# Performance work log

Hardware: AMD Instinct MI355X
Metric: run time of the kernel (lower is better)

Reference implementation:

```python
import jax, jax.numpy as jnp
import numpy as np

# Dimensions: classic FORCE setup (Sussillo & Abbott / tension EchoStateNetwork)
N = 1024      # force_layer.units (reservoir size)
T = 128       # timesteps (train_step loops over x.shape[1])
I_DIM = 16    # input dimension
O_DIM = 8     # output dimension
DT = 0.1      # leak rate of the reservoir cell
ALPHA_P = 1.0 # P initialized to alpha_P * I (keras.initializers.Identity(gain=alpha_P))


def setup_inputs() -> dict:
    key = jax.random.key(0)
    k0, k1, k2, k3, k4 = jax.random.split(key, 5)
    x = jax.random.normal(k0, (1, T, I_DIM), dtype=jnp.float32)
    y = jax.random.normal(k1, (1, T, O_DIM), dtype=jnp.float32)
    Win = jax.random.normal(k2, (I_DIM, N), dtype=jnp.float32) * (1.0 / np.sqrt(I_DIM))
    # spectral-radius-style scaling keeps the reservoir in the chaotic-edge regime
    Wrec = jax.random.normal(k3, (N, N), dtype=jnp.float32) * (1.5 / np.sqrt(N))
    Wfb = jax.random.normal(k4, (O_DIM, N), dtype=jnp.float32)
    wO = jnp.zeros((N, O_DIM), dtype=jnp.float32)        # output_kernel starts at 0
    P = ALPHA_P * jnp.eye(N, dtype=jnp.float32)           # P_output = alpha_P * I
    return {"x": x, "y": y, "Win": Win, "Wrec": Wrec, "Wfb": Wfb, "wO": wO, "P": P}


def reference(x, y, Win, Wrec, Wfb, wO, P):
    """FORCEModel.train_step: per-timestep RNN forward + RLS (FORCE) update.

    Per step t (batch is fixed to 1, so states are vectors):
      a_t = (1-dt)*a_{t-1} + dt*(h_{t-1}@Wrec + x_t@Win + z_{t-1}@Wfb)
      h_t = tanh(a_t);  z_t = h_t @ wO   (output uses wO *before* this step's update)
      RLS (pseudogradient_P, SGD lr=1 => P -= dP):
        k = P @ h;  c = 1/(1 + h.k);  P <- P - c * k k^T
      then (pseudogradient_wO with the *updated* P, matching apply_gradients order):
        e = z - y_t;  wO <- wO - (P @ h) e^T
    Returns the sequence of pre-update outputs z_t, shape (T, O_DIM).
    """
    xs = x[0]  # (T, I_DIM)
    ys = y[0]  # (T, O_DIM)
    a0 = jnp.zeros((N,), dtype=x.dtype)
    h0 = jnp.tanh(a0)
    z0 = jnp.zeros((O_DIM,), dtype=x.dtype)

    def step(carry, inp):
        a, h, z, P_t, wO_t = carry
        xt, yt = inp
        a = (1.0 - DT) * a + DT * (h @ Wrec + xt @ Win + z @ Wfb)
        h = jnp.tanh(a)
        z = h @ wO_t                           # (O_DIM,)
        # pseudogradient_P: rank-1 Sherman-Morrison style update of P
        k = P_t @ h                            # (N,)
        c = 1.0 / (1.0 + jnp.dot(h, k))
        P_t = P_t - c * jnp.outer(k, k)
        # pseudogradient_wO with updated P
        wO_t = wO_t - jnp.outer(P_t @ h, z - yt)
        return (a, h, z, P_t, wO_t), z

    (_, _, _, P_f, wO_f), zs = jax.lax.scan(step, (a0, h0, z0, P, wO), (xs, ys))
    return zs  # (T, O_DIM)
```

## Files before the change

### kernel.cpp

```cpp
#include <hip/hip_runtime.h>
#include <math.h>


#define NN   1024
#define TT   128
#define IDIM 16
#define ODIM 8
#define NBLK 64
#define NTHR 256
#define JPB  16
#define GST  (TT + 8)
#define NGRP 8
#define WREC_LD (NN + 4)

#define AL(p)    __hip_atomic_load((p), __ATOMIC_RELAXED, __HIP_MEMORY_SCOPE_AGENT)
#define AS(p, v) __hip_atomic_store((p), (v), __ATOMIC_RELAXED, __HIP_MEMORY_SCOPE_AGENT)

struct WS {
  unsigned arrive[NGRP][32];
  unsigned master[32];
  unsigned rel[NGRP][32];
  float hglob[2][NN];
  float gpart[2][NBLK][GST];
};

__global__ __launch_bounds__(NTHR, 1) void force_rls_kernel(
    const float* __restrict__ x, const float* __restrict__ y,
    const float* __restrict__ Win, const float* __restrict__ Wrec,
    const float* __restrict__ Wfb, float* __restrict__ out, WS* ws)
{
  const int tid  = threadIdx.x;
  const int bid  = blockIdx.x;
  const int lane = tid & 63;
  const int wv   = tid >> 6;
  const int j0   = bid * JPB;
  const int jj   = tid & 15;
  const int qq   = tid >> 4;
  const int grp  = bid >> 3;

  __shared__ float Wsl_t[JPB][WREC_LD];
  __shared__ float Ksl[TT][JPB];
  __shared__ float XW[TT][JPB];
  __shared__ float Ybuf[TT][ODIM];
  __shared__ float Ebuf[TT][ODIM];
  __shared__ float hfull[NN];
  __shared__ float cbuf[TT], dbuf[TT];
  __shared__ float Wfb_s[ODIM][JPB];
  __shared__ float Winsl[IDIM][JPB];
  __shared__ float redK[16][JPB], redM[16][JPB];
  __shared__ float redG[2][TT];
  __shared__ float hcb[JPB], abuf[JPB], zbuf[ODIM];
  __shared__ float red2[4];
  __shared__ float sHH;

  for (int m = 0; m < (NN * JPB) / NTHR; ++m) {
    int e = m * NTHR + tid;
    int r = e >> 4, j = e & 15;
    Wsl_t[j][r] = Wrec[(size_t)r * NN + j0 + j];
  }
  { int i = tid >> 4, j = tid & 15; Winsl[i][j] = Win[i * NN + j0 + j]; }
  if (tid < ODIM * JPB) { int o = tid >> 4, j = tid & 15; Wfb_s[o][j] = Wfb[o * NN + j0 + j]; }
  for (int m = 0; m < (TT * ODIM) / NTHR; ++m) {
    int e = m * NTHR + tid; Ybuf[e >> 3][e & 7] = y[e];
  }
  if (tid < JPB) abuf[tid] = 0.f;
  if (tid < ODIM) zbuf[tid] = 0.f;
  __syncthreads();
  for (int m = 0; m < (TT * JPB) / NTHR; ++m) {
    int e = m * NTHR + tid; int t = e >> 4, j = e & 15;
    float s = 0.f;
#pragma unroll
    for (int i = 0; i < IDIM; ++i) s += x[t * IDIM + i] * Winsl[i][j];
    XW[t][j] = s;
  }
  __syncthreads();

  for (int t = 0; t < TT; ++t) {
    const int p = t & 1;

    if (t >= 1) {
      const float* hg = ws->hglob[p ^ 1];
#pragma unroll
      for (int m = 0; m < NN / NTHR; ++m) {
        int idx = m * NTHR + tid;
        hfull[idx] = AL(&hg[idx]);
      }
    }
    __syncthreads();

    float kp = 0.f;
    if (t >= 1) {
      for (int s = qq; s < t - 1; s += 16) kp -= dbuf[s] * Ksl[s][jj];
    }
    redK[qq][jj] = kp;

    float mp = 0.f;
    if (t >= 1) {
      const float4* hf4 = (const float4*)hfull;
#pragma unroll
      for (int i = 0; i < 16; ++i) {
        const int rb = (i << 6) + (qq << 2);
        const float4 w  = *(const float4*)&Wsl_t[jj][rb];
        const float4 hv = hf4[rb >> 2];
        mp += hv.x * w.x + hv.y * w.y + hv.z * w.z + hv.w * w.w;
      }
    }
    redM[qq][jj] = mp;
    __syncthreads();

    if (tid < JPB) {
      const int j = tid;
      if (t >= 1) {
        float kv = hfull[j0 + j];
#pragma unroll
        for (int q = 0; q < 16; ++q) kv += redK[q][j];
        Ksl[t - 1][j] = kv;
      }
      float acc = 0.f;
#pragma unroll
      for (int q = 0; q < 16; ++q) acc += redM[q][j];
      float fb = 0.f;
#pragma unroll
      for (int o = 0; o < ODIM; ++o) fb += zbuf[o] * Wfb_s[o][j];
      float a = 0.9f * abuf[j] + 0.1f * (acc + XW[t][j] + fb);
      abuf[j] = a;
      float h = tanhf(a);
      hcb[j] = h;
      AS(&ws->hglob[p][j0 + j], h);
    }
    __syncthreads();

    if (tid <= t) {
      float gp = 0.f;
      if (tid < t) {
#pragma unroll
        for (int j = 0; j < JPB; ++j) gp += Ksl[tid][j] * hcb[j];
      } else {
#pragma unroll
        for (int j = 0; j < JPB; ++j) gp += hcb[j] * hcb[j];
      }
      AS(&ws->gpart[p][bid][tid], gp);
    }

    __syncthreads();
    if (tid == 0) {
      asm volatile("s_waitcnt vmcnt(0)" ::: "memory");
      const unsigned tgt = (unsigned)(t + 1) * 8u;
      unsigned r = __hip_atomic_fetch_add(&ws->arrive[grp][0], 1u,
                      __ATOMIC_RELAXED, __HIP_MEMORY_SCOPE_AGENT);
      if (r == tgt - 1u) {
        unsigned m = __hip_atomic_fetch_add(&ws->master[0], 1u,
                        __ATOMIC_RELAXED, __HIP_MEMORY_SCOPE_AGENT);
        if (m == tgt - 1u) {
#pragma unroll
          for (int g = 0; g < NGRP; ++g) AS(&ws->rel[g][0], (unsigned)(t + 1));
        }
      }
      while (AL(&ws->rel[grp][0]) < (unsigned)(t + 1))
        __builtin_amdgcn_s_sleep(8);
      asm volatile("s_waitcnt vmcnt(0)" ::: "memory");
    }
    __syncthreads();

    {
      const int sF = tid & 127;
      const int hf = tid >> 7;
      float gp = 0.f;
      if (sF <= t) {
        const int b0 = hf * 32;
#pragma unroll
        for (int b = 0; b < 32; ++b) gp += AL(&ws->gpart[p][b0 + b][sF]);
      }
      redG[hf][sF] = gp;
    }
    __syncthreads();
    float dval = 0.f, gval = 0.f;
    if (tid <= t) {
      float g = redG[0][tid] + redG[1][tid];
      gval = g;
      if (tid < t) { dval = cbuf[tid] * g; dbuf[tid] = dval; }
      else sHH = g;
    }
    float s1p = dval * gval;
    s1p += __shfl_xor(s1p, 1, 64);
    s1p += __shfl_xor(s1p, 2, 64);
    s1p += __shfl_xor(s1p, 4, 64);
    s1p += __shfl_xor(s1p, 8, 64);
    s1p += __shfl_xor(s1p, 16, 64);
    s1p += __shfl_xor(s1p, 32, 64);
    if (lane == 0) red2[wv] = s1p;
    __syncthreads();
    if (tid == 0) {
      float s1 = red2[0] + red2[1] + red2[2] + red2[3];
      cbuf[t] = 1.f / (1.f + sHH - s1);
    }
    if (wv == 0) {
      const int o = lane & 7, gr8 = lane >> 3;
      float zp = 0.f;
      for (int s = gr8; s < t; s += 8) zp += dbuf[s] * Ebuf[s][o];
      zp += __shfl_xor(zp, 8, 64);
      zp += __shfl_xor(zp, 16, 64);
      zp += __shfl_xor(zp, 32, 64);
      if (lane < 8) {
        float z = -zp;
        zbuf[o] = z;
        Ebuf[t][o] = z - Ybuf[t][o];
        if (bid == 0) out[t * ODIM + o] = z;
      }
    }
    __syncthreads();
  }
}

extern "C" void kernel_launch(void* const* d_in, const int* in_sizes, int n_in,
                              void* d_out, int out_size, void* d_ws, size_t ws_size,
                              hipStream_t stream) {
  const float* x    = (const float*)d_in[0];
  const float* y    = (const float*)d_in[1];
  const float* Win  = (const float*)d_in[2];
  const float* Wrec = (const float*)d_in[3];
  const float* Wfb  = (const float*)d_in[4];
  float* out = (float*)d_out;
  WS* ws = (WS*)d_ws;

  hipMemsetAsync(d_ws, 0, sizeof(unsigned) * 32 * (NGRP * 2 + 1), stream);
  force_rls_kernel<<<NBLK, NTHR, 0, stream>>>(x, y, Win, Wrec, Wfb, out, ws);
}
```

Baseline: 806.7 us.

## Merge grid barriers into one per step via flag array and deferred reduction

```diff
diff --git a/kernel.cpp b/kernel.cpp
--- a/kernel.cpp
+++ b/kernel.cpp
@@ -10,16 +10,13 @@
 #define NTHR 256
 #define JPB  16
 #define GST  (TT + 8)
-#define NGRP 8
 #define WREC_LD (NN + 4)
 
 #define AL(p)    __hip_atomic_load((p), __ATOMIC_RELAXED, __HIP_MEMORY_SCOPE_AGENT)
 #define AS(p, v) __hip_atomic_store((p), (v), __ATOMIC_RELAXED, __HIP_MEMORY_SCOPE_AGENT)
 
 struct WS {
-  unsigned arrive[NGRP][32];
-  unsigned master[32];
-  unsigned rel[NGRP][32];
+  unsigned flag[64];
   float hglob[2][NN];
   float gpart[2][NBLK][GST];
 };
@@ -36,7 +33,8 @@
   const int j0   = bid * JPB;
   const int jj   = tid & 15;
   const int qq   = tid >> 4;
-  const int grp  = bid >> 3;
+  const int sF   = tid & 127;
+  const int hf   = tid >> 7;
 
   __shared__ float Wsl_t[JPB][WREC_LD];
   __shared__ float Ksl[TT][JPB];
@@ -80,19 +78,23 @@
 
     if (t >= 1) {
       const float* hg = ws->hglob[p ^ 1];
-#pragma unroll
-      for (int m = 0; m < NN / NTHR; ++m) {
-        int idx = m * NTHR + tid;
-        hfull[idx] = AL(&hg[idx]);
-      }
-    }
-    __syncthreads();
-
-    float kp = 0.f;
-    if (t >= 1) {
-      for (int s = qq; s < t - 1; s += 16) kp -= dbuf[s] * Ksl[s][jj];
-    }
-    redK[qq][jj] = kp;
+      float hr0 = AL(&hg[tid]);
+      float hr1 = AL(&hg[NTHR + tid]);
+      float hr2 = AL(&hg[2 * NTHR + tid]);
+      float hr3 = AL(&hg[3 * NTHR + tid]);
+      float ga = 0.f;
+      if (sF < t) {
+        const float* gq = &ws->gpart[p ^ 1][hf * 32][sF];
+#pragma unroll
+        for (int b = 0; b < 32; ++b) ga += AL(&gq[b * GST]);
+      }
+      hfull[tid]            = hr0;
+      hfull[NTHR + tid]     = hr1;
+      hfull[2 * NTHR + tid] = hr2;
+      hfull[3 * NTHR + tid] = hr3;
+      redG[hf][sF] = ga;
+    }
+    __syncthreads();
 
     float mp = 0.f;
     if (t >= 1) {
@@ -106,79 +108,12 @@
       }
     }
     redM[qq][jj] = mp;
-    __syncthreads();
-
-    if (tid < JPB) {
-      const int j = tid;
-      if (t >= 1) {
-        float kv = hfull[j0 + j];
-#pragma unroll
-        for (int q = 0; q < 16; ++q) kv += redK[q][j];
-        Ksl[t - 1][j] = kv;
-      }
-      float acc = 0.f;
-#pragma unroll
-      for (int q = 0; q < 16; ++q) acc += redM[q][j];
-      float fb = 0.f;
-#pragma unroll
-      for (int o = 0; o < ODIM; ++o) fb += zbuf[o] * Wfb_s[o][j];
-      float a = 0.9f * abuf[j] + 0.1f * (acc + XW[t][j] + fb);
-      abuf[j] = a;
-      float h = tanhf(a);
-      hcb[j] = h;
-      AS(&ws->hglob[p][j0 + j], h);
-    }
-    __syncthreads();
-
-    if (tid <= t) {
-      float gp = 0.f;
-      if (tid < t) {
-#pragma unroll
-        for (int j = 0; j < JPB; ++j) gp += Ksl[tid][j] * hcb[j];
-      } else {
-#pragma unroll
-        for (int j = 0; j < JPB; ++j) gp += hcb[j] * hcb[j];
-      }
-      AS(&ws->gpart[p][bid][tid], gp);
-    }
-
-    __syncthreads();
-    if (tid == 0) {
-      asm volatile("s_waitcnt vmcnt(0)" ::: "memory");
-      const unsigned tgt = (unsigned)(t + 1) * 8u;
-      unsigned r = __hip_atomic_fetch_add(&ws->arrive[grp][0], 1u,
-                      __ATOMIC_RELAXED, __HIP_MEMORY_SCOPE_AGENT);
-      if (r == tgt - 1u) {
-        unsigned m = __hip_atomic_fetch_add(&ws->master[0], 1u,
-                        __ATOMIC_RELAXED, __HIP_MEMORY_SCOPE_AGENT);
-        if (m == tgt - 1u) {
-#pragma unroll
-          for (int g = 0; g < NGRP; ++g) AS(&ws->rel[g][0], (unsigned)(t + 1));
-        }
-      }
-      while (AL(&ws->rel[grp][0]) < (unsigned)(t + 1))
-        __builtin_amdgcn_s_sleep(8);
-      asm volatile("s_waitcnt vmcnt(0)" ::: "memory");
-    }
-    __syncthreads();
-
-    {
-      const int sF = tid & 127;
-      const int hf = tid >> 7;
-      float gp = 0.f;
-      if (sF <= t) {
-        const int b0 = hf * 32;
-#pragma unroll
-        for (int b = 0; b < 32; ++b) gp += AL(&ws->gpart[p][b0 + b][sF]);
-      }
-      redG[hf][sF] = gp;
-    }
-    __syncthreads();
+
     float dval = 0.f, gval = 0.f;
-    if (tid <= t) {
+    if (t >= 1 && tid <= t - 1) {
       float g = redG[0][tid] + redG[1][tid];
       gval = g;
-      if (tid < t) { dval = cbuf[tid] * g; dbuf[tid] = dval; }
+      if (tid < t - 1) { dval = cbuf[tid] * g; dbuf[tid] = dval; }
       else sHH = g;
     }
     float s1p = dval * gval;
@@ -190,25 +125,104 @@
     s1p += __shfl_xor(s1p, 32, 64);
     if (lane == 0) red2[wv] = s1p;
     __syncthreads();
+
+    if (t >= 1) {
+      if (tid == 0) {
+        float s1 = red2[0] + red2[1] + red2[2] + red2[3];
+        cbuf[t - 1] = 1.f / (1.f + sHH - s1);
+      }
+      if (wv == 0) {
+        const int o = lane & 7, gr8 = lane >> 3;
+        float zp = 0.f;
+        for (int s = gr8; s < t - 1; s += 8) zp += dbuf[s] * Ebuf[s][o];
+        zp += __shfl_xor(zp, 8, 64);
+        zp += __shfl_xor(zp, 16, 64);
+        zp += __shfl_xor(zp, 32, 64);
+        if (lane < 8) {
+          float z = -zp;
+          zbuf[o] = z;
+          Ebuf[t - 1][o] = z - Ybuf[t - 1][o];
+          if (bid == 0) out[(t - 1) * ODIM + o] = z;
+        }
+      }
+    }
+    float kp = 0.f;
+    if (t >= 2) {
+      for (int s = qq; s < t - 1; s += 16) kp -= dbuf[s] * Ksl[s][jj];
+    }
+    redK[qq][jj] = kp;
+    __syncthreads();
+
+    if (tid < JPB) {
+      const int j = tid;
+      if (t >= 1) {
+        float kv = hfull[j0 + j];
+#pragma unroll
+        for (int q = 0; q < 16; ++q) kv += redK[q][j];
+        Ksl[t - 1][j] = kv;
+      }
+      float acc = 0.f;
+#pragma unroll
+      for (int q = 0; q < 16; ++q) acc += redM[q][j];
+      float fb = 0.f;
+#pragma unroll
+      for (int o = 0; o < ODIM; ++o) fb += zbuf[o] * Wfb_s[o][j];
+      float a = 0.9f * abuf[j] + 0.1f * (acc + XW[t][j] + fb);
+      abuf[j] = a;
+      float h = tanhf(a);
+      hcb[j] = h;
+      AS(&ws->hglob[p][j0 + j], h);
+    }
+    __syncthreads();
+
+    if (tid <= t) {
+      float gp = 0.f;
+      if (tid < t) {
+#pragma unroll
+        for (int j = 0; j < JPB; ++j) gp += Ksl[tid][j] * hcb[j];
+      } else {
+#pragma unroll
+        for (int j = 0; j < JPB; ++j) gp += hcb[j] * hcb[j];
+      }
+      AS(&ws->gpart[p][bid][tid], gp);
+    }
+    __syncthreads();
+
     if (tid == 0) {
-      float s1 = red2[0] + red2[1] + red2[2] + red2[3];
-      cbuf[t] = 1.f / (1.f + sHH - s1);
-    }
+      asm volatile("s_waitcnt vmcnt(0)" ::: "memory");
+      AS(&ws->flag[bid], (unsigned)(t + 1));
+    }
+    if (wv == 0) {
+      const unsigned tgt = (unsigned)(t + 1);
+      unsigned v = AL(&ws->flag[lane]);
+      while (!__all((int)(v >= tgt))) {
+        __builtin_amdgcn_s_sleep(2);
+        v = AL(&ws->flag[lane]);
+      }
+    }
+    __syncthreads();
+  }
+
+  if (bid == 0) {
+    float ga = 0.f;
+    if (sF < TT - 1) {
+      const float* gq = &ws->gpart[(TT - 1) & 1][hf * 32][sF];
+#pragma unroll
+      for (int b = 0; b < 32; ++b) ga += AL(&gq[b * GST]);
+    }
+    redG[hf][sF] = ga;
+    __syncthreads();
+    if (tid < TT - 1) dbuf[tid] = cbuf[tid] * (redG[0][tid] + redG[1][tid]);
+    __syncthreads();
     if (wv == 0) {
       const int o = lane & 7, gr8 = lane >> 3;
       float zp = 0.f;
-      for (int s = gr8; s < t; s += 8) zp += dbuf[s] * Ebuf[s][o];
+      for (int s = gr8; s < TT - 1; s += 8) zp += dbuf[s] * Ebuf[s][o];
       zp += __shfl_xor(zp, 8, 64);
       zp += __shfl_xor(zp, 16, 64);
       zp += __shfl_xor(zp, 32, 64);
-      if (lane < 8) {
-        float z = -zp;
-        zbuf[o] = z;
-        Ebuf[t][o] = z - Ybuf[t][o];
-        if (bid == 0) out[t * ODIM + o] = z;
-      }
-    }
-    __syncthreads();
+      if (lane < 8) out[(TT - 1) * ODIM + o] = -zp;
+    }
   }
 }
 
@@ -223,6 +237,6 @@
   float* out = (float*)d_out;
   WS* ws = (WS*)d_ws;
 
-  hipMemsetAsync(d_ws, 0, sizeof(unsigned) * 32 * (NGRP * 2 + 1), stream);
+  hipMemsetAsync(d_ws, 0, sizeof(unsigned) * 64, stream);
   force_rls_kernel<<<NBLK, NTHR, 0, stream>>>(x, y, Win, Wrec, Wfb, out, ws);
 }
```

Measured after the change: 813.1 us. No clear change (+0.8%).
